# Kernel optimization log

Hardware: AMD Instinct MI355X
Metric: run time of the kernel (lower is better)

The kernel has to match this reference:

```python
import jax, jax.numpy as jnp
import numpy as np

N_NODES = 50000
N_EDGES = 800000
IN_FEATS = 64
OUT_FEATS = 64
EDGE_DIM = 8


def setup_inputs() -> dict:
    key = jax.random.key(0)
    k1, k2, k3, k4, k5 = jax.random.split(key, 5)
    node_feat = jax.random.normal(k1, (N_NODES, IN_FEATS), dtype=jnp.float32)
    edge_feat = jax.random.normal(k2, (N_EDGES, EDGE_DIM), dtype=jnp.float32)
    W = jax.random.normal(k3, (OUT_FEATS, IN_FEATS), dtype=jnp.float32) * (1.0 / np.sqrt(IN_FEATS))
    b = jnp.zeros((OUT_FEATS,), dtype=jnp.float32)
    src = jax.random.randint(k4, (N_EDGES,), 0, N_NODES, dtype=jnp.int64 if jax.config.jax_enable_x64 else jnp.int32)
    dst = jax.random.randint(k5, (N_EDGES,), 0, N_NODES, dtype=jnp.int64 if jax.config.jax_enable_x64 else jnp.int32)
    return {"node_feat": node_feat, "edge_feat": edge_feat, "W": W, "b": b,
            "src": src, "dst": dst}


def reference(node_feat, edge_feat, W, b, src, dst):
    # EfConv forward with aggregate='sum', node_feat.shape[1] == in_feats.
    n_nodes = node_feat.shape[0]
    edge_dim = edge_feat.shape[1]
    h_src = node_feat[src]  # [E, in_feats] gather once, reused for every slice
    aggs = []
    for k in range(edge_dim):  # small fixed loop over edge feature slices
        m = h_src * edge_feat[:, k:k + 1]                      # u_mul_e: [E, in_feats]
        aggs.append(jax.ops.segment_sum(m, dst, num_segments=n_nodes))
    agg = jnp.stack(aggs, axis=1)                              # [N, edge_dim, in_feats]
    # per-slice shared linear, then concat along feature dim
    out = jnp.einsum('nki,oi->nko', agg, W) + b                # [N, edge_dim, out_feats]
    return out.reshape(n_nodes, edge_dim * W.shape[0])         # [N, edge_dim*out_feats]
```

## Files before the change

kernel.cpp:

```cpp
#include <hip/hip_runtime.h>


#define FEATS 64
#define EDGE_DIM 8

__global__ void __launch_bounds__(256) transform_kernel(
    const float* __restrict__ nf, const float* __restrict__ W,
    float* __restrict__ t, int* __restrict__ deg, int n_nodes)
{
    __shared__ float sWt[FEATS * 65];
    __shared__ float srow[4][FEATS];
    const int tid = threadIdx.x;

    #pragma unroll
    for (int base = 0; base < FEATS * FEATS; base += 256) {
        int idx = base + tid;
        sWt[(idx & 63) * 65 + (idx >> 6)] = W[idx];
    }

    const int r = tid >> 6;
    const int o = tid & 63;
    const int node = blockIdx.x * 4 + r;
    if (node < n_nodes) srow[r][o] = nf[(long)node * FEATS + o];
    if (tid < 4) {
        int zn = blockIdx.x * 4 + tid;
        if (zn < n_nodes) deg[zn] = 0;
    }
    __syncthreads();

    if (node >= n_nodes) return;
    float sum = 0.f;
    #pragma unroll
    for (int i = 0; i < FEATS; i++)
        sum += srow[r][i] * sWt[i * 65 + o];
    t[(long)node * FEATS + o] = sum;
}

__global__ void __launch_bounds__(256) hist_kernel(
    const int* __restrict__ dst, int* __restrict__ deg, int n_edges)
{
    int i = (blockIdx.x * 256 + threadIdx.x) * 4;
    if (i + 3 < n_edges) {
        int4 d = *(const int4*)(dst + i);
        atomicAdd(&deg[d.x], 1);
        atomicAdd(&deg[d.y], 1);
        atomicAdd(&deg[d.z], 1);
        atomicAdd(&deg[d.w], 1);
    } else {
        for (int e = i; e < n_edges; e++) atomicAdd(&deg[dst[e]], 1);
    }
}

__global__ void __launch_bounds__(256) partials_kernel(
    const int* __restrict__ deg, int* __restrict__ partials, int n)
{
    __shared__ int s[256];
    int i = blockIdx.x * 256 + threadIdx.x;
    s[threadIdx.x] = (i < n) ? deg[i] : 0;
    __syncthreads();
    for (int off = 128; off > 0; off >>= 1) {
        if (threadIdx.x < off) s[threadIdx.x] += s[threadIdx.x + off];
        __syncthreads();
    }
    if (threadIdx.x == 0) partials[blockIdx.x] = s[0];
}

__global__ void __launch_bounds__(256) scan_partials_kernel(
    const int* __restrict__ partials, int* __restrict__ pscan, int nb)
{
    __shared__ int s[256];
    int tid = threadIdx.x;
    s[tid] = (tid < nb) ? partials[tid] : 0;
    for (int off = 1; off < 256; off <<= 1) {
        __syncthreads();
        int x = (tid >= off) ? s[tid - off] : 0;
        __syncthreads();
        s[tid] += x;
    }
    __syncthreads();
    pscan[tid] = (tid == 0) ? 0 : s[tid - 1];
}

__global__ void __launch_bounds__(256) scan_addback_kernel(
    const int* __restrict__ deg, const int* __restrict__ pscan,
    int* __restrict__ offsets, int* __restrict__ cursor,
    int n, int n_edges)
{
    __shared__ int s[256];
    int tid = threadIdx.x;
    int i = blockIdx.x * 256 + tid;
    int v = (i < n) ? deg[i] : 0;
    s[tid] = v;
    for (int off = 1; off < 256; off <<= 1) {
        __syncthreads();
        int x = (tid >= off) ? s[tid - off] : 0;
        __syncthreads();
        s[tid] += x;
    }
    __syncthreads();
    if (i < n) {
        int excl = pscan[blockIdx.x] + s[tid] - v;
        offsets[i] = excl;
        cursor[i]  = excl;
    }
    if (blockIdx.x == 0 && tid == 0) offsets[n] = n_edges;
}

__global__ void __launch_bounds__(256) permute_ef_kernel(
    const int* __restrict__ src, const int* __restrict__ dst,
    const float4* __restrict__ ef4, int* __restrict__ cursor,
    int* __restrict__ src_s, float4* __restrict__ efs4, int n_edges)
{
    int e = blockIdx.x * 256 + threadIdx.x;
    if (e >= n_edges) return;
    int pos = atomicAdd(&cursor[dst[e]], 1);
    src_s[pos] = src[e];
    float4 a = ef4[2l * e], c = ef4[2l * e + 1];
    efs4[2l * pos] = a;
    efs4[2l * pos + 1] = c;
}

__global__ void __launch_bounds__(256) permute_kernel(
    const int* __restrict__ src, const int* __restrict__ dst,
    int* __restrict__ cursor, int* __restrict__ src_s, int* __restrict__ perm,
    int n_edges)
{
    int e = blockIdx.x * 256 + threadIdx.x;
    if (e >= n_edges) return;
    int pos = atomicAdd(&cursor[dst[e]], 1);
    src_s[pos] = src[e];
    perm[pos] = e;
}

__global__ void __launch_bounds__(256) aggregate_stream_kernel(
    const float* __restrict__ t, const float4* __restrict__ efs4,
    const int* __restrict__ src_s, const int* __restrict__ offsets,
    const float* __restrict__ b, float* __restrict__ out, int n_nodes)
{
    int node = (blockIdx.x * 256 + threadIdx.x) >> 6;
    int o = threadIdx.x & 63;
    if (node >= n_nodes) return;

    int beg = offsets[node];
    int end = offsets[node + 1];
    float acc[EDGE_DIM];
    #pragma unroll
    for (int k = 0; k < EDGE_DIM; k++) acc[k] = 0.f;

    int j = beg;
    for (; j + 3 < end; j += 4) {
        int s0 = src_s[j],     s1 = src_s[j + 1];
        int s2 = src_s[j + 2], s3 = src_s[j + 3];
        float tv0 = t[(long)s0 * FEATS + o];
        float tv1 = t[(long)s1 * FEATS + o];
        float tv2 = t[(long)s2 * FEATS + o];
        float tv3 = t[(long)s3 * FEATS + o];
        float4 a0 = efs4[2l * j],     a1 = efs4[2l * j + 1];
        float4 b0 = efs4[2l * j + 2], b1 = efs4[2l * j + 3];
        float4 c0 = efs4[2l * j + 4], c1 = efs4[2l * j + 5];
        float4 d0 = efs4[2l * j + 6], d1 = efs4[2l * j + 7];
        acc[0] += a0.x * tv0 + b0.x * tv1 + c0.x * tv2 + d0.x * tv3;
        acc[1] += a0.y * tv0 + b0.y * tv1 + c0.y * tv2 + d0.y * tv3;
        acc[2] += a0.z * tv0 + b0.z * tv1 + c0.z * tv2 + d0.z * tv3;
        acc[3] += a0.w * tv0 + b0.w * tv1 + c0.w * tv2 + d0.w * tv3;
        acc[4] += a1.x * tv0 + b1.x * tv1 + c1.x * tv2 + d1.x * tv3;
        acc[5] += a1.y * tv0 + b1.y * tv1 + c1.y * tv2 + d1.y * tv3;
        acc[6] += a1.z * tv0 + b1.z * tv1 + c1.z * tv2 + d1.z * tv3;
        acc[7] += a1.w * tv0 + b1.w * tv1 + c1.w * tv2 + d1.w * tv3;
    }
    for (; j < end; j++) {
        int s0 = src_s[j];
        float tv0 = t[(long)s0 * FEATS + o];
        float4 a0 = efs4[2l * j], a1 = efs4[2l * j + 1];
        acc[0] += a0.x * tv0; acc[1] += a0.y * tv0;
        acc[2] += a0.z * tv0; acc[3] += a0.w * tv0;
        acc[4] += a1.x * tv0; acc[5] += a1.y * tv0;
        acc[6] += a1.z * tv0; acc[7] += a1.w * tv0;
    }

    float bo = b[o];
    float* op = out + (long)node * (EDGE_DIM * FEATS) + o;
    #pragma unroll
    for (int k = 0; k < EDGE_DIM; k++)
        __builtin_nontemporal_store(acc[k] + bo, op + k * FEATS);
}

__global__ void __launch_bounds__(256) aggregate_kernel(
    const float* __restrict__ t, const float* __restrict__ ef,
    const int* __restrict__ src_s, const int* __restrict__ perm,
    const int* __restrict__ offsets, const float* __restrict__ b,
    float* __restrict__ out, int n_nodes)
{
    int node = (blockIdx.x * 256 + threadIdx.x) >> 6;
    int o = threadIdx.x & 63;
    if (node >= n_nodes) return;

    int beg = offsets[node];
    int end = offsets[node + 1];
    float acc[EDGE_DIM];
    #pragma unroll
    for (int k = 0; k < EDGE_DIM; k++) acc[k] = 0.f;

    int j = beg;
    for (; j + 1 < end; j += 2) {
        int e0 = perm[j], e1 = perm[j + 1];
        int s0 = src_s[j], s1 = src_s[j + 1];
        float tv0 = t[(long)s0 * FEATS + o];
        float tv1 = t[(long)s1 * FEATS + o];
        const float4* p0 = (const float4*)(ef + (long)e0 * EDGE_DIM);
        const float4* p1 = (const float4*)(ef + (long)e1 * EDGE_DIM);
        float4 a0 = p0[0], a1 = p0[1];
        float4 c0 = p1[0], c1 = p1[1];
        acc[0] += a0.x * tv0 + c0.x * tv1;
        acc[1] += a0.y * tv0 + c0.y * tv1;
        acc[2] += a0.z * tv0 + c0.z * tv1;
        acc[3] += a0.w * tv0 + c0.w * tv1;
        acc[4] += a1.x * tv0 + c1.x * tv1;
        acc[5] += a1.y * tv0 + c1.y * tv1;
        acc[6] += a1.z * tv0 + c1.z * tv1;
        acc[7] += a1.w * tv0 + c1.w * tv1;
    }
    if (j < end) {
        int e0 = perm[j];
        int s0 = src_s[j];
        float tv0 = t[(long)s0 * FEATS + o];
        const float4* p0 = (const float4*)(ef + (long)e0 * EDGE_DIM);
        float4 a0 = p0[0], a1 = p0[1];
        acc[0] += a0.x * tv0; acc[1] += a0.y * tv0;
        acc[2] += a0.z * tv0; acc[3] += a0.w * tv0;
        acc[4] += a1.x * tv0; acc[5] += a1.y * tv0;
        acc[6] += a1.z * tv0; acc[7] += a1.w * tv0;
    }

    float bo = b[o];
    float* op = out + (long)node * (EDGE_DIM * FEATS) + o;
    #pragma unroll
    for (int k = 0; k < EDGE_DIM; k++)
        __builtin_nontemporal_store(acc[k] + bo, op + k * FEATS);
}

extern "C" void kernel_launch(void* const* d_in, const int* in_sizes, int n_in,
                              void* d_out, int out_size, void* d_ws, size_t ws_size,
                              hipStream_t stream) {
    const float* node_feat = (const float*)d_in[0];
    const float* edge_feat = (const float*)d_in[1];
    const float* W         = (const float*)d_in[2];
    const float* b         = (const float*)d_in[3];
    const int*   src       = (const int*)d_in[4];
    const int*   dst       = (const int*)d_in[5];
    float* out = (float*)d_out;

    const int n_nodes = in_sizes[0] / FEATS;
    const int n_edges = in_sizes[4];
    const int nb_nodes = (n_nodes + 255) / 256;
    const int nb_edges = (n_edges + 255) / 256;

    int* w = (int*)d_ws;
    float* t      = (float*)w;
    int* deg      = w + (long)n_nodes * FEATS;
    int* offsets  = deg + n_nodes;
    int* cursor   = offsets + n_nodes + 1;
    int* partials = cursor + n_nodes;
    int* pscan    = partials + 256;
    int* src_s    = pscan + 256;
    int* tail     = src_s + n_edges;

    const size_t need_efs = ((size_t)(tail - w) + (size_t)n_edges * EDGE_DIM) * 4;
    const bool use_efs = (ws_size >= need_efs) &&
                         ((((uintptr_t)edge_feat) & 15) == 0) &&
                         ((((uintptr_t)tail) & 15) == 0);

    transform_kernel<<<(n_nodes + 3) / 4, 256, 0, stream>>>(node_feat, W, t, deg, n_nodes);
    hist_kernel<<<(n_edges + 1023) / 1024, 256, 0, stream>>>(dst, deg, n_edges);
    partials_kernel<<<nb_nodes, 256, 0, stream>>>(deg, partials, n_nodes);
    scan_partials_kernel<<<1, 256, 0, stream>>>(partials, pscan, nb_nodes);
    scan_addback_kernel<<<nb_nodes, 256, 0, stream>>>(deg, pscan, offsets, cursor,
                                                      n_nodes, n_edges);

    const long total_ag = (long)n_nodes * 64;
    if (use_efs) {
        permute_ef_kernel<<<nb_edges, 256, 0, stream>>>(
            src, dst, (const float4*)edge_feat, cursor, src_s, (float4*)tail, n_edges);
        aggregate_stream_kernel<<<(int)((total_ag + 255) / 256), 256, 0, stream>>>(
            t, (const float4*)tail, src_s, offsets, b, out, n_nodes);
    } else {
        permute_kernel<<<nb_edges, 256, 0, stream>>>(src, dst, cursor, src_s, tail, n_edges);
        aggregate_kernel<<<(int)((total_ag + 255) / 256), 256, 0, stream>>>(
            t, edge_feat, src_s, tail, offsets, b, out, n_nodes);
    }
}
```

Before: 333.3 us.

## Merge CSR build into one cooperative kernel with grid syncs

```diff
diff --git a/kernel.cpp b/kernel.cpp
--- a/kernel.cpp
+++ b/kernel.cpp
@@ -1,139 +1,151 @@
 #include <hip/hip_runtime.h>
+#include <hip/hip_cooperative_groups.h>
+
+namespace cg = cooperative_groups;
 
 
 #define FEATS 64
 #define EDGE_DIM 8
 
-__global__ void __launch_bounds__(256) transform_kernel(
+typedef float nfloat4 __attribute__((ext_vector_type(4)));
+
+__global__ void __launch_bounds__(256, 4) build_kernel(
     const float* __restrict__ nf, const float* __restrict__ W,
-    float* __restrict__ t, int* __restrict__ deg, int n_nodes)
-{
+    const float* __restrict__ ef, const int* __restrict__ src,
+    const int* __restrict__ dst,
+    float* __restrict__ t, int* __restrict__ deg, int* __restrict__ offsets,
+    int* __restrict__ cursor, int* __restrict__ partials, int* __restrict__ pscan,
+    int* __restrict__ src_s, int* __restrict__ perm, float* __restrict__ ef_s,
+    int n_nodes, int n_edges, int use_efs)
+{
+    cg::grid_group grid = cg::this_grid();
     __shared__ float sWt[FEATS * 65];
     __shared__ float srow[4][FEATS];
+    __shared__ int sscan[256];
+    __shared__ int srun;
     const int tid = threadIdx.x;
+    const int nb = gridDim.x;
 
     #pragma unroll
     for (int base = 0; base < FEATS * FEATS; base += 256) {
         int idx = base + tid;
         sWt[(idx & 63) * 65 + (idx >> 6)] = W[idx];
     }
-
-    const int r = tid >> 6;
-    const int o = tid & 63;
-    const int node = blockIdx.x * 4 + r;
-    if (node < n_nodes) srow[r][o] = nf[(long)node * FEATS + o];
-    if (tid < 4) {
-        int zn = blockIdx.x * 4 + tid;
-        if (zn < n_nodes) deg[zn] = 0;
-    }
+    for (int i = blockIdx.x * 256 + tid; i < n_nodes; i += nb * 256) deg[i] = 0;
     __syncthreads();
 
-    if (node >= n_nodes) return;
-    float sum = 0.f;
-    #pragma unroll
-    for (int i = 0; i < FEATS; i++)
-        sum += srow[r][i] * sWt[i * 65 + o];
-    t[(long)node * FEATS + o] = sum;
-}
-
-__global__ void __launch_bounds__(256) hist_kernel(
-    const int* __restrict__ dst, int* __restrict__ deg, int n_edges)
-{
-    int i = (blockIdx.x * 256 + threadIdx.x) * 4;
-    if (i + 3 < n_edges) {
-        int4 d = *(const int4*)(dst + i);
-        atomicAdd(&deg[d.x], 1);
-        atomicAdd(&deg[d.y], 1);
-        atomicAdd(&deg[d.z], 1);
-        atomicAdd(&deg[d.w], 1);
+    const int r = tid >> 6, o = tid & 63;
+    const int ngroups = (n_nodes + 3) >> 2;
+    for (int g = blockIdx.x; g < ngroups; g += nb) {
+        int node = g * 4 + r;
+        if (node < n_nodes) srow[r][o] = nf[(long)node * FEATS + o];
+        __syncthreads();
+        if (node < n_nodes) {
+            float sum = 0.f;
+            #pragma unroll
+            for (int i = 0; i < FEATS; i++) sum += srow[r][i] * sWt[i * 65 + o];
+            t[(long)node * FEATS + o] = sum;
+        }
+        __syncthreads();
+    }
+
+    __threadfence();
+    grid.sync();
+
+    const int nq = n_edges >> 2;
+    for (int q = blockIdx.x * 256 + tid; q < nq; q += nb * 256) {
+        int4 d4 = ((const int4*)dst)[q];
+        atomicAdd(&deg[d4.x], 1); atomicAdd(&deg[d4.y], 1);
+        atomicAdd(&deg[d4.z], 1); atomicAdd(&deg[d4.w], 1);
+    }
+    if (blockIdx.x == 0 && tid < (n_edges & 3)) atomicAdd(&deg[dst[nq * 4 + tid]], 1);
+
+    __threadfence();
+    grid.sync();
+
+    const int ntiles = (n_nodes + 255) >> 8;
+    for (int tl = blockIdx.x; tl < ntiles; tl += nb) {
+        int i = tl * 256 + tid;
+        sscan[tid] = (i < n_nodes) ? deg[i] : 0;
+        __syncthreads();
+        for (int off = 128; off > 0; off >>= 1) {
+            if (tid < off) sscan[tid] += sscan[tid + off];
+            __syncthreads();
+        }
+        if (tid == 0) partials[tl] = sscan[0];
+        __syncthreads();
+    }
+
+    __threadfence();
+    grid.sync();
+
+    if (blockIdx.x == 0) {
+        if (tid == 0) srun = 0;
+        __syncthreads();
+        for (int base = 0; base < ntiles; base += 256) {
+            int idx = base + tid;
+            int v = (idx < ntiles) ? partials[idx] : 0;
+            sscan[tid] = v;
+            for (int off = 1; off < 256; off <<= 1) {
+                __syncthreads();
+                int x = (tid >= off) ? sscan[tid - off] : 0;
+                __syncthreads();
+                sscan[tid] += x;
+            }
+            __syncthreads();
+            if (idx < ntiles) pscan[idx] = srun + sscan[tid] - v;
+            __syncthreads();
+            if (tid == 0) srun += sscan[255];
+            __syncthreads();
+        }
+    }
+
+    __threadfence();
+    grid.sync();
+
+    for (int tl = blockIdx.x; tl < ntiles; tl += nb) {
+        int i = tl * 256 + tid;
+        int v = (i < n_nodes) ? deg[i] : 0;
+        sscan[tid] = v;
+        for (int off = 1; off < 256; off <<= 1) {
+            __syncthreads();
+            int x = (tid >= off) ? sscan[tid - off] : 0;
+            __syncthreads();
+            sscan[tid] += x;
+        }
+        __syncthreads();
+        if (i < n_nodes) {
+            int excl = pscan[tl] + sscan[tid] - v;
+            offsets[i] = excl;
+            cursor[i]  = excl;
+        }
+        __syncthreads();
+    }
+    if (blockIdx.x == 0 && tid == 0) offsets[n_nodes] = n_edges;
+
+    __threadfence();
+    grid.sync();
+
+    if (use_efs) {
+        for (int e = blockIdx.x * 256 + tid; e < n_edges; e += nb * 256) {
+            int pos = atomicAdd(&cursor[dst[e]], 1);
+            src_s[pos] = src[e];
+            const nfloat4* efe = (const nfloat4*)(ef + (long)e * EDGE_DIM);
+            nfloat4 a = efe[0], c = efe[1];
+            nfloat4* dp = (nfloat4*)(ef_s + (long)pos * EDGE_DIM);
+            dp[0] = a; dp[1] = c;
+        }
     } else {
-        for (int e = i; e < n_edges; e++) atomicAdd(&deg[dst[e]], 1);
-    }
-}
-
-__global__ void __launch_bounds__(256) partials_kernel(
-    const int* __restrict__ deg, int* __restrict__ partials, int n)
-{
-    __shared__ int s[256];
-    int i = blockIdx.x * 256 + threadIdx.x;
-    s[threadIdx.x] = (i < n) ? deg[i] : 0;
-    __syncthreads();
-    for (int off = 128; off > 0; off >>= 1) {
-        if (threadIdx.x < off) s[threadIdx.x] += s[threadIdx.x + off];
-        __syncthreads();
-    }
-    if (threadIdx.x == 0) partials[blockIdx.x] = s[0];
-}
-
-__global__ void __launch_bounds__(256) scan_partials_kernel(
-    const int* __restrict__ partials, int* __restrict__ pscan, int nb)
-{
-    __shared__ int s[256];
-    int tid = threadIdx.x;
-    s[tid] = (tid < nb) ? partials[tid] : 0;
-    for (int off = 1; off < 256; off <<= 1) {
-        __syncthreads();
-        int x = (tid >= off) ? s[tid - off] : 0;
-        __syncthreads();
-        s[tid] += x;
-    }
-    __syncthreads();
-    pscan[tid] = (tid == 0) ? 0 : s[tid - 1];
-}
-
-__global__ void __launch_bounds__(256) scan_addback_kernel(
-    const int* __restrict__ deg, const int* __restrict__ pscan,
-    int* __restrict__ offsets, int* __restrict__ cursor,
-    int n, int n_edges)
-{
-    __shared__ int s[256];
-    int tid = threadIdx.x;
-    int i = blockIdx.x * 256 + tid;
-    int v = (i < n) ? deg[i] : 0;
-    s[tid] = v;
-    for (int off = 1; off < 256; off <<= 1) {
-        __syncthreads();
-        int x = (tid >= off) ? s[tid - off] : 0;
-        __syncthreads();
-        s[tid] += x;
-    }
-    __syncthreads();
-    if (i < n) {
-        int excl = pscan[blockIdx.x] + s[tid] - v;
-        offsets[i] = excl;
-        cursor[i]  = excl;
-    }
-    if (blockIdx.x == 0 && tid == 0) offsets[n] = n_edges;
-}
-
-__global__ void __launch_bounds__(256) permute_ef_kernel(
-    const int* __restrict__ src, const int* __restrict__ dst,
-    const float4* __restrict__ ef4, int* __restrict__ cursor,
-    int* __restrict__ src_s, float4* __restrict__ efs4, int n_edges)
-{
-    int e = blockIdx.x * 256 + threadIdx.x;
-    if (e >= n_edges) return;
-    int pos = atomicAdd(&cursor[dst[e]], 1);
-    src_s[pos] = src[e];
-    float4 a = ef4[2l * e], c = ef4[2l * e + 1];
-    efs4[2l * pos] = a;
-    efs4[2l * pos + 1] = c;
-}
-
-__global__ void __launch_bounds__(256) permute_kernel(
-    const int* __restrict__ src, const int* __restrict__ dst,
-    int* __restrict__ cursor, int* __restrict__ src_s, int* __restrict__ perm,
-    int n_edges)
-{
-    int e = blockIdx.x * 256 + threadIdx.x;
-    if (e >= n_edges) return;
-    int pos = atomicAdd(&cursor[dst[e]], 1);
-    src_s[pos] = src[e];
-    perm[pos] = e;
+        for (int e = blockIdx.x * 256 + tid; e < n_edges; e += nb * 256) {
+            int pos = atomicAdd(&cursor[dst[e]], 1);
+            src_s[pos] = src[e];
+            perm[pos] = e;
+        }
+    }
 }
 
 __global__ void __launch_bounds__(256) aggregate_stream_kernel(
-    const float* __restrict__ t, const float4* __restrict__ efs4,
+    const float* __restrict__ t, const float* __restrict__ efs,
     const int* __restrict__ src_s, const int* __restrict__ offsets,
     const float* __restrict__ b, float* __restrict__ out, int n_nodes)
 {
@@ -147,35 +159,35 @@
     #pragma unroll
     for (int k = 0; k < EDGE_DIM; k++) acc[k] = 0.f;
 
+    const nfloat4* efs4 = (const nfloat4*)efs;
+
     int j = beg;
-    for (; j + 3 < end; j += 4) {
-        int s0 = src_s[j],     s1 = src_s[j + 1];
-        int s2 = src_s[j + 2], s3 = src_s[j + 3];
-        float tv0 = t[(long)s0 * FEATS + o];
-        float tv1 = t[(long)s1 * FEATS + o];
-        float tv2 = t[(long)s2 * FEATS + o];
-        float tv3 = t[(long)s3 * FEATS + o];
-        float4 a0 = efs4[2l * j],     a1 = efs4[2l * j + 1];
-        float4 b0 = efs4[2l * j + 2], b1 = efs4[2l * j + 3];
-        float4 c0 = efs4[2l * j + 4], c1 = efs4[2l * j + 5];
-        float4 d0 = efs4[2l * j + 6], d1 = efs4[2l * j + 7];
-        acc[0] += a0.x * tv0 + b0.x * tv1 + c0.x * tv2 + d0.x * tv3;
-        acc[1] += a0.y * tv0 + b0.y * tv1 + c0.y * tv2 + d0.y * tv3;
-        acc[2] += a0.z * tv0 + b0.z * tv1 + c0.z * tv2 + d0.z * tv3;
-        acc[3] += a0.w * tv0 + b0.w * tv1 + c0.w * tv2 + d0.w * tv3;
-        acc[4] += a1.x * tv0 + b1.x * tv1 + c1.x * tv2 + d1.x * tv3;
-        acc[5] += a1.y * tv0 + b1.y * tv1 + c1.y * tv2 + d1.y * tv3;
-        acc[6] += a1.z * tv0 + b1.z * tv1 + c1.z * tv2 + d1.z * tv3;
-        acc[7] += a1.w * tv0 + b1.w * tv1 + c1.w * tv2 + d1.w * tv3;
+    for (; j + 7 < end; j += 8) {
+        int sidx[8];
+        float tv[8];
+        #pragma unroll
+        for (int u = 0; u < 8; u++) sidx[u] = src_s[j + u];
+        #pragma unroll
+        for (int u = 0; u < 8; u++) tv[u] = t[(long)sidx[u] * FEATS + o];
+        #pragma unroll
+        for (int u = 0; u < 8; u++) {
+            nfloat4 e0 = __builtin_nontemporal_load(&efs4[2l * (j + u)]);
+            nfloat4 e1 = __builtin_nontemporal_load(&efs4[2l * (j + u) + 1]);
+            acc[0] += e0.x * tv[u]; acc[1] += e0.y * tv[u];
+            acc[2] += e0.z * tv[u]; acc[3] += e0.w * tv[u];
+            acc[4] += e1.x * tv[u]; acc[5] += e1.y * tv[u];
+            acc[6] += e1.z * tv[u]; acc[7] += e1.w * tv[u];
+        }
     }
     for (; j < end; j++) {
         int s0 = src_s[j];
         float tv0 = t[(long)s0 * FEATS + o];
-        float4 a0 = efs4[2l * j], a1 = efs4[2l * j + 1];
-        acc[0] += a0.x * tv0; acc[1] += a0.y * tv0;
-        acc[2] += a0.z * tv0; acc[3] += a0.w * tv0;
-        acc[4] += a1.x * tv0; acc[5] += a1.y * tv0;
-        acc[6] += a1.z * tv0; acc[7] += a1.w * tv0;
+        nfloat4 e0 = __builtin_nontemporal_load(&efs4[2l * j]);
+        nfloat4 e1 = __builtin_nontemporal_load(&efs4[2l * j + 1]);
+        acc[0] += e0.x * tv0; acc[1] += e0.y * tv0;
+        acc[2] += e0.z * tv0; acc[3] += e0.w * tv0;
+        acc[4] += e1.x * tv0; acc[5] += e1.y * tv0;
+        acc[6] += e1.z * tv0; acc[7] += e1.w * tv0;
     }
 
     float bo = b[o];
@@ -239,6 +251,127 @@
         __builtin_nontemporal_store(acc[k] + bo, op + k * FEATS);
 }
 
+__global__ void __launch_bounds__(256) transform_kernel(
+    const float* __restrict__ nf, const float* __restrict__ W,
+    float* __restrict__ t, int* __restrict__ deg, int n_nodes)
+{
+    __shared__ float sWt[FEATS * 65];
+    __shared__ float srow[4][FEATS];
+    const int tid = threadIdx.x;
+    #pragma unroll
+    for (int base = 0; base < FEATS * FEATS; base += 256) {
+        int idx = base + tid;
+        sWt[(idx & 63) * 65 + (idx >> 6)] = W[idx];
+    }
+    const int r = tid >> 6, o = tid & 63;
+    const int node = blockIdx.x * 4 + r;
+    if (node < n_nodes) srow[r][o] = nf[(long)node * FEATS + o];
+    if (tid < 4) {
+        int zn = blockIdx.x * 4 + tid;
+        if (zn < n_nodes) deg[zn] = 0;
+    }
+    __syncthreads();
+    if (node >= n_nodes) return;
+    float sum = 0.f;
+    #pragma unroll
+    for (int i = 0; i < FEATS; i++) sum += srow[r][i] * sWt[i * 65 + o];
+    t[(long)node * FEATS + o] = sum;
+}
+
+__global__ void __launch_bounds__(256) hist_kernel(
+    const int* __restrict__ dst, int* __restrict__ deg, int n_edges)
+{
+    int i = (blockIdx.x * 256 + threadIdx.x) * 4;
+    if (i + 3 < n_edges) {
+        int4 d = *(const int4*)(dst + i);
+        atomicAdd(&deg[d.x], 1); atomicAdd(&deg[d.y], 1);
+        atomicAdd(&deg[d.z], 1); atomicAdd(&deg[d.w], 1);
+    } else {
+        for (int e = i; e < n_edges; e++) atomicAdd(&deg[dst[e]], 1);
+    }
+}
+
+__global__ void __launch_bounds__(256) partials_kernel(
+    const int* __restrict__ deg, int* __restrict__ partials, int n)
+{
+    __shared__ int s[256];
+    int i = blockIdx.x * 256 + threadIdx.x;
+    s[threadIdx.x] = (i < n) ? deg[i] : 0;
+    __syncthreads();
+    for (int off = 128; off > 0; off >>= 1) {
+        if (threadIdx.x < off) s[threadIdx.x] += s[threadIdx.x + off];
+        __syncthreads();
+    }
+    if (threadIdx.x == 0) partials[blockIdx.x] = s[0];
+}
+
+__global__ void __launch_bounds__(256) scan_partials_kernel(
+    const int* __restrict__ partials, int* __restrict__ pscan, int nb)
+{
+    __shared__ int s[256];
+    int tid = threadIdx.x;
+    s[tid] = (tid < nb) ? partials[tid] : 0;
+    for (int off = 1; off < 256; off <<= 1) {
+        __syncthreads();
+        int x = (tid >= off) ? s[tid - off] : 0;
+        __syncthreads();
+        s[tid] += x;
+    }
+    __syncthreads();
+    pscan[tid] = (tid == 0) ? 0 : s[tid - 1];
+}
+
+__global__ void __launch_bounds__(256) scan_addback_kernel(
+    const int* __restrict__ deg, const int* __restrict__ pscan,
+    int* __restrict__ offsets, int* __restrict__ cursor, int n, int n_edges)
+{
+    __shared__ int s[256];
+    int tid = threadIdx.x;
+    int i = blockIdx.x * 256 + tid;
+    int v = (i < n) ? deg[i] : 0;
+    s[tid] = v;
+    for (int off = 1; off < 256; off <<= 1) {
+        __syncthreads();
+        int x = (tid >= off) ? s[tid - off] : 0;
+        __syncthreads();
+        s[tid] += x;
+    }
+    __syncthreads();
+    if (i < n) {
+        int excl = pscan[blockIdx.x] + s[tid] - v;
+        offsets[i] = excl;
+        cursor[i]  = excl;
+    }
+    if (blockIdx.x == 0 && tid == 0) offsets[n] = n_edges;
+}
+
+__global__ void __launch_bounds__(256) permute_ef_kernel(
+    const int* __restrict__ src, const int* __restrict__ dst,
+    const float* __restrict__ ef, int* __restrict__ cursor,
+    int* __restrict__ src_s, float* __restrict__ efs, int n_edges)
+{
+    int e = blockIdx.x * 256 + threadIdx.x;
+    if (e >= n_edges) return;
+    int pos = atomicAdd(&cursor[dst[e]], 1);
+    src_s[pos] = src[e];
+    const nfloat4* efe = (const nfloat4*)(ef + (long)e * EDGE_DIM);
+    nfloat4 a = efe[0], c = efe[1];
+    nfloat4* dp = (nfloat4*)(efs + (long)pos * EDGE_DIM);
+    dp[0] = a; dp[1] = c;
+}
+
+__global__ void __launch_bounds__(256) permute_kernel(
+    const int* __restrict__ src, const int* __restrict__ dst,
+    int* __restrict__ cursor, int* __restrict__ src_s, int* __restrict__ perm,
+    int n_edges)
+{
+    int e = blockIdx.x * 256 + threadIdx.x;
+    if (e >= n_edges) return;
+    int pos = atomicAdd(&cursor[dst[e]], 1);
+    src_s[pos] = src[e];
+    perm[pos] = e;
+}
+
 extern "C" void kernel_launch(void* const* d_in, const int* in_sizes, int n_in,
                               void* d_out, int out_size, void* d_ws, size_t ws_size,
                               hipStream_t stream) {
@@ -250,42 +383,65 @@
     const int*   dst       = (const int*)d_in[5];
     float* out = (float*)d_out;
 
-    const int n_nodes = in_sizes[0] / FEATS;
-    const int n_edges = in_sizes[4];
-    const int nb_nodes = (n_nodes + 255) / 256;
-    const int nb_edges = (n_edges + 255) / 256;
-
-    int* w = (int*)d_ws;
-    float* t      = (float*)w;
-    int* deg      = w + (long)n_nodes * FEATS;
-    int* offsets  = deg + n_nodes;
-    int* cursor   = offsets + n_nodes + 1;
-    int* partials = cursor + n_nodes;
-    int* pscan    = partials + 256;
-    int* src_s    = pscan + 256;
-    int* tail     = src_s + n_edges;
-
-    const size_t need_efs = ((size_t)(tail - w) + (size_t)n_edges * EDGE_DIM) * 4;
-    const bool use_efs = (ws_size >= need_efs) &&
-                         ((((uintptr_t)edge_feat) & 15) == 0) &&
-                         ((((uintptr_t)tail) & 15) == 0);
-
-    transform_kernel<<<(n_nodes + 3) / 4, 256, 0, stream>>>(node_feat, W, t, deg, n_nodes);
-    hist_kernel<<<(n_edges + 1023) / 1024, 256, 0, stream>>>(dst, deg, n_edges);
-    partials_kernel<<<nb_nodes, 256, 0, stream>>>(deg, partials, n_nodes);
-    scan_partials_kernel<<<1, 256, 0, stream>>>(partials, pscan, nb_nodes);
-    scan_addback_kernel<<<nb_nodes, 256, 0, stream>>>(deg, pscan, offsets, cursor,
-                                                      n_nodes, n_edges);
+    int n_nodes = in_sizes[0] / FEATS;
+    int n_edges = in_sizes[4];
+
+    char* p = (char*)d_ws;
+    auto take = [&](size_t bytes) -> char* {
+        char* r = p; p += (bytes + 63) & ~(size_t)63; return r;
+    };
+    float* t      = (float*)take((size_t)n_nodes * FEATS * 4);
+    int* deg      = (int*)take((size_t)n_nodes * 4);
+    int* offsets  = (int*)take(((size_t)n_nodes + 1) * 4);
+    int* cursor   = (int*)take((size_t)n_nodes * 4);
+    int* partials = (int*)take(4096 * 4);
+    int* pscan    = (int*)take(4096 * 4);
+    int* src_s    = (int*)take((size_t)n_edges * 4);
+    int* perm     = (int*)take((size_t)n_edges * 4);
+    float* ef_s   = (float*)take((size_t)n_edges * EDGE_DIM * 4);
+    size_t used_efs = (size_t)(p - (char*)d_ws);
+
+    int use_efs = (used_efs <= ws_size) ? 1 : 0;
+
+    int maxPerCU = 0;
+    hipError_t occ_err = hipOccupancyMaxActiveBlocksPerMultiprocessor(
+        &maxPerCU, build_kernel, 256, 0);
+    int grid = (occ_err == hipSuccess && maxPerCU > 0) ? maxPerCU * 256 : 256;
+    if (grid > 1024) grid = 1024;
+
+    void* args[] = {
+        (void*)&node_feat, (void*)&W, (void*)&edge_feat, (void*)&src, (void*)&dst,
+        (void*)&t, (void*)&deg, (void*)&offsets, (void*)&cursor,
+        (void*)&partials, (void*)&pscan, (void*)&src_s, (void*)&perm, (void*)&ef_s,
+        (void*)&n_nodes, (void*)&n_edges, (void*)&use_efs
+    };
+    hipError_t lerr = hipLaunchCooperativeKernel(
+        (const void*)build_kernel, dim3(grid), dim3(256), args, 0, stream);
+
+    if (lerr != hipSuccess) {
+        const int nb_nodes = (n_nodes + 255) / 256;
+        const int nb_edges = (n_edges + 255) / 256;
+        transform_kernel<<<(n_nodes + 3) / 4, 256, 0, stream>>>(node_feat, W, t, deg, n_nodes);
+        hist_kernel<<<(n_edges + 1023) / 1024, 256, 0, stream>>>(dst, deg, n_edges);
+        partials_kernel<<<nb_nodes, 256, 0, stream>>>(deg, partials, n_nodes);
+        scan_partials_kernel<<<1, 256, 0, stream>>>(partials, pscan, nb_nodes);
+        scan_addback_kernel<<<nb_nodes, 256, 0, stream>>>(deg, pscan, offsets, cursor,
+                                                          n_nodes, n_edges);
+        if (use_efs) {
+            permute_ef_kernel<<<nb_edges, 256, 0, stream>>>(
+                src, dst, edge_feat, cursor, src_s, ef_s, n_edges);
+        } else {
+            permute_kernel<<<nb_edges, 256, 0, stream>>>(src, dst, cursor, src_s, perm, n_edges);
+        }
+    }
 
     const long total_ag = (long)n_nodes * 64;
+    const int ag_blocks = (int)((total_ag + 255) / 256);
     if (use_efs) {
-        permute_ef_kernel<<<nb_edges, 256, 0, stream>>>(
-            src, dst, (const float4*)edge_feat, cursor, src_s, (float4*)tail, n_edges);
-        aggregate_stream_kernel<<<(int)((total_ag + 255) / 256), 256, 0, stream>>>(
-            t, (const float4*)tail, src_s, offsets, b, out, n_nodes);
+        aggregate_stream_kernel<<<ag_blocks, 256, 0, stream>>>(
+            t, ef_s, src_s, offsets, b, out, n_nodes);
     } else {
-        permute_kernel<<<nb_edges, 256, 0, stream>>>(src, dst, cursor, src_s, tail, n_edges);
-        aggregate_kernel<<<(int)((total_ag + 255) / 256), 256, 0, stream>>>(
-            t, edge_feat, src_s, tail, offsets, b, out, n_nodes);
-    }
-}
+        aggregate_kernel<<<ag_blocks, 256, 0, stream>>>(
+            t, edge_feat, src_s, perm, offsets, b, out, n_nodes);
+    }
+}
```

New measurement: 1.122 ms. +236.6%, slower.
